# Performance work log

Measured on AMD Instinct MI355X. Metric: run time of the kernel, lower is better.

## Reference

```python
import jax, jax.numpy as jnp
import numpy as np


def setup_inputs() -> dict:
    key = jax.random.key(0)
    k1, k2, k3, k4 = jax.random.split(key, 4)
    N, E, F, H = 100000, 1600000, 128, 128
    x = jax.random.normal(k1, (N, F), dtype=jnp.float32)
    edge_index = jax.random.randint(k2, (2, E), 0, N, dtype=jnp.int64)
    W1 = jax.random.normal(k3, (F, H), dtype=jnp.float32) * (1.0 / np.sqrt(F))
    b1 = jnp.zeros((H,), dtype=jnp.float32)
    W2 = jax.random.normal(k4, (H, H), dtype=jnp.float32) * (1.0 / np.sqrt(H))
    b2 = jnp.zeros((H,), dtype=jnp.float32)
    return {"x": x, "edge_index": edge_index, "W1": W1, "b1": b1, "W2": W2, "b2": b2}


def reference(x, edge_index, W1, b1, W2, b2):
    # Two-layer cached GCN: norm is computed once (cached) and reused by both layers.
    N = x.shape[0]
    loops = jnp.arange(N, dtype=edge_index.dtype)
    src = jnp.concatenate([edge_index[0], loops])  # add self-loops
    dst = jnp.concatenate([edge_index[1], loops])
    # symmetric GCN normalization: deg^-1/2[src] * deg^-1/2[dst]
    deg = jax.ops.segment_sum(jnp.ones_like(dst, dtype=x.dtype), dst, num_segments=N)
    dinv = jnp.where(deg > 0, jax.lax.rsqrt(deg), 0.0)
    norm = dinv[src] * dinv[dst]  # [E+N]

    def conv(h, W, b):
        h = h @ W  # dense transform before sparse aggregate (cheaper: out_dim small)
        msg = norm[:, None] * h[src]  # gather + scale
        return jax.ops.segment_sum(msg, dst, num_segments=N) + b

    h = jax.nn.relu(conv(x, W1, b1))
    # dropout is identity in eval mode (deterministic reference)
    return conv(h, W2, b2)
```

## Files before the change

kernel.cpp:

```cpp
#include <hip/hip_runtime.h>


#define BKT_SHIFT 7
#define BKT_NODES 128
#define CH 8192
#define MAXBKT 1024

typedef _Float16 half4v __attribute__((ext_vector_type(4)));
typedef _Float16 half8v __attribute__((ext_vector_type(8)));
typedef float float4v __attribute__((ext_vector_type(4)));

__global__ __launch_bounds__(256) void k_bincount(const int* __restrict__ dst,
                                                  int* __restrict__ bcnt, int E, int nbkt) {
    __shared__ int sh[MAXBKT];
    for (int i = threadIdx.x; i < nbkt; i += 256) sh[i] = 0;
    __syncthreads();
    for (long long e = (long long)blockIdx.x * 256 + threadIdx.x; e < E;
         e += (long long)gridDim.x * 256)
        atomicAdd(&sh[dst[e] >> BKT_SHIFT], 1);
    __syncthreads();
    for (int i = threadIdx.x; i < nbkt; i += 256)
        if (sh[i]) atomicAdd(&bcnt[i], sh[i]);
}

__global__ __launch_bounds__(1024) void k_bscan(const int* __restrict__ bcnt,
                                                int* __restrict__ bofs,
                                                int* __restrict__ bcur, int nbkt, int E) {
    __shared__ int sh[1024];
    int t = threadIdx.x;
    int v = (t < nbkt) ? bcnt[t] : 0;
    int x = v;
    sh[t] = x;
    __syncthreads();
    for (int o = 1; o < 1024; o <<= 1) {
        int y = (t >= o) ? sh[t - o] : 0;
        __syncthreads();
        x += y;
        sh[t] = x;
        __syncthreads();
    }
    if (t < nbkt) { bofs[t] = x - v; bcur[t] = x - v; }
    if (t == 0) bofs[nbkt] = E;
}

__global__ __launch_bounds__(256) void k_binfill(const int* __restrict__ src,
                                                 const int* __restrict__ dst,
                                                 int* __restrict__ bcur,
                                                 unsigned* __restrict__ recs,
                                                 int E, int nbkt) {
    __shared__ unsigned stage[CH];
    __shared__ unsigned short stageb[CH];
    __shared__ int cnt[MAXBKT];
    __shared__ int base[MAXBKT];
    const int t = threadIdx.x;
    const long long c0 = (long long)blockIdx.x * CH;

    for (int i = t; i < nbkt; i += 256) cnt[i] = 0;
    __syncthreads();

    for (int k = 0; k < CH / 256; k++) {
        int i = k * 256 + t;
        long long e = c0 + i;
        if (e < E) {
            int d = dst[e];
            int b = d >> BKT_SHIFT;
            stage[i] = ((unsigned)(d & (BKT_NODES - 1)) << 17) | (unsigned)src[e];
            stageb[i] = (unsigned short)b;
            atomicAdd(&cnt[b], 1);
        }
    }
    __syncthreads();

    for (int i = t; i < nbkt; i += 256) {
        int c = cnt[i];
        base[i] = c ? atomicAdd(&bcur[i], c) : 0;
        cnt[i] = 0;
    }
    __syncthreads();

    for (int k = 0; k < CH / 256; k++) {
        int i = k * 256 + t;
        if (c0 + i < E) {
            int b = stageb[i];
            int p = base[b] + atomicAdd(&cnt[b], 1);
            recs[p] = stage[i];
        }
    }
}

__global__ __launch_bounds__(256) void k_deg_bins(const unsigned* __restrict__ recs,
                                                  const int* __restrict__ bofs,
                                                  int* __restrict__ deg, int n) {
    __shared__ int cnt[BKT_NODES];
    const int b = blockIdx.x, t = threadIdx.x;
    if (t < BKT_NODES) cnt[t] = 0;
    __syncthreads();
    const int beg = bofs[b], end = bofs[b + 1];
    for (int j = beg + t; j < end; j += 256)
        atomicAdd(&cnt[recs[j] >> 17], 1);
    __syncthreads();
    const int d0 = b << BKT_SHIFT;
    if (t < BKT_NODES && d0 + t < n) deg[d0 + t] = cnt[t];
}

__global__ void k_scan1(const int* __restrict__ deg, float* __restrict__ dinv,
                        int* __restrict__ ofs, int* __restrict__ sums, int n) {
    __shared__ int sh[256];
    const int t = threadIdx.x;
    const int i = blockIdx.x * 256 + t;
    int v = (i < n) ? deg[i] : 0;
    if (i < n) dinv[i] = rsqrtf((float)v + 1.0f);
    int x = v;
    sh[t] = x;
    __syncthreads();
    for (int o = 1; o < 256; o <<= 1) {
        int y = (t >= o) ? sh[t - o] : 0;
        __syncthreads();
        x += y;
        sh[t] = x;
        __syncthreads();
    }
    if (i < n) ofs[i] = x - v;
    if (t == 255) sums[blockIdx.x] = x;
}

__global__ void k_scan2(int* __restrict__ sums, int nb) {
    __shared__ int sh[512];
    const int t = threadIdx.x;
    int carry = 0;
    for (int base = 0; base < nb; base += 512) {
        int i = base + t;
        int v = (i < nb) ? sums[i] : 0;
        int x = v;
        sh[t] = x;
        __syncthreads();
        for (int o = 1; o < 512; o <<= 1) {
            int y = (t >= o) ? sh[t - o] : 0;
            __syncthreads();
            x += y;
            sh[t] = x;
            __syncthreads();
        }
        if (i < nb) sums[i] = x - v + carry;
        int tot = sh[511];
        __syncthreads();
        carry += tot;
    }
}

__global__ void k_scan3(int* __restrict__ ofs, const int* __restrict__ sums, int n, int E) {
    int i = blockIdx.x * 256 + threadIdx.x;
    if (i < n) ofs[i] += sums[blockIdx.x];
    if (i == 0) ofs[n] = E;
}

__global__ __launch_bounds__(256) void k_fill_bins(const unsigned* __restrict__ recs,
                                                   const int* __restrict__ bofs,
                                                   const int* __restrict__ ofs,
                                                   int* __restrict__ col, int n) {
    __shared__ int cur[BKT_NODES];
    const int b = blockIdx.x, t = threadIdx.x;
    const int d0 = b << BKT_SHIFT;
    if (t < BKT_NODES) cur[t] = (d0 + t < n) ? ofs[d0 + t] : 0;
    __syncthreads();
    const int beg = bofs[b], end = bofs[b + 1];
    for (int j = beg + t; j < end; j += 256) {
        unsigned r = recs[j];
        int p = atomicAdd(&cur[r >> 17], 1);
        col[p] = (int)(r & 0x1FFFF);
    }
}

__global__ __launch_bounds__(256) void k_wt(const float* __restrict__ W,
                                            _Float16* __restrict__ Wt) {
    int i = blockIdx.x * 256 + threadIdx.x;
    int k = i >> 7, c = i & 127;
    Wt[c * 128 + k] = (_Float16)W[k * 128 + c];
}

__global__ __launch_bounds__(256, 2) void k_gemm_mfma(const float* __restrict__ in,
                                                      const _Float16* __restrict__ Wt,
                                                      const float* __restrict__ dinv,
                                                      _Float16* __restrict__ out,
                                                      int n, int relu_in) {
    __shared__ _Float16 Al[64][136];
    __shared__ _Float16 Bl[128][136];
    const int t = threadIdx.x;
    const int row0 = blockIdx.x * 64;
    int nr = n - row0;
    if (nr > 64) nr = 64;

    for (int i = t; i < 128 * 16; i += 256) {
        int r = i >> 4, c8 = i & 15;
        *(half8v*)&Bl[r][c8 * 8] = *(const half8v*)&Wt[r * 128 + c8 * 8];
    }
    for (int i = t; i < nr * 32; i += 256) {
        int r = i >> 5, c4 = i & 31;
        float4 v = *(const float4*)&in[(size_t)(row0 + r) * 128 + c4 * 4];
        if (relu_in) {
            v.x = fmaxf(v.x, 0.f); v.y = fmaxf(v.y, 0.f);
            v.z = fmaxf(v.z, 0.f); v.w = fmaxf(v.w, 0.f);
        }
        half4v hv;
        hv[0] = (_Float16)v.x; hv[1] = (_Float16)v.y;
        hv[2] = (_Float16)v.z; hv[3] = (_Float16)v.w;
        *(half4v*)&Al[r][c4 * 4] = hv;
    }
    __syncthreads();

    const int wave = t >> 6;
    const int lane = t & 63;
    const int m0 = wave * 16;
    const int ml = lane & 15;
    const int quad = lane >> 4;

    float4v acc[8] = {};
#pragma unroll
    for (int kc = 0; kc < 4; kc++) {
        half8v a = *(const half8v*)&Al[m0 + ml][kc * 32 + quad * 8];
#pragma unroll
        for (int nt = 0; nt < 8; nt++) {
            half8v b = *(const half8v*)&Bl[nt * 16 + ml][kc * 32 + quad * 8];
            acc[nt] = __builtin_amdgcn_mfma_f32_16x16x32_f16(a, b, acc[nt], 0, 0, 0);
        }
    }

#pragma unroll
    for (int reg = 0; reg < 4; reg++) {
        int r = m0 + quad * 4 + reg;
        if (r < nr) {
            float dv = dinv[row0 + r];
#pragma unroll
            for (int nt = 0; nt < 8; nt++)
                out[(size_t)(row0 + r) * 128 + nt * 16 + ml] =
                    (_Float16)(acc[nt][reg] * dv);
        }
    }
}

__global__ __launch_bounds__(256) void k_agg_csr(const int* __restrict__ ofs,
                                                 const int* __restrict__ col,
                                                 const float* __restrict__ dinv,
                                                 const half4v* __restrict__ ts,
                                                 const float* __restrict__ bias,
                                                 float* __restrict__ out, int n) {
    int gid = blockIdx.x * 256 + threadIdx.x;
    int row = gid >> 5;
    int lane = gid & 31;
    if (row >= n) return;

    float dd = dinv[row];
    int beg = ofs[row];
    int end = ofs[row + 1];

    half4v sv = ts[(size_t)row * 32 + lane];
    float4 acc = make_float4((float)sv[0], (float)sv[1], (float)sv[2], (float)sv[3]);

    int j = beg;
    for (; j + 3 < end; j += 4) {
        int s0 = col[j], s1 = col[j + 1], s2 = col[j + 2], s3 = col[j + 3];
        half4v v0 = ts[(size_t)s0 * 32 + lane];
        half4v v1 = ts[(size_t)s1 * 32 + lane];
        half4v v2 = ts[(size_t)s2 * 32 + lane];
        half4v v3 = ts[(size_t)s3 * 32 + lane];
        acc.x += (float)v0[0] + (float)v1[0] + (float)v2[0] + (float)v3[0];
        acc.y += (float)v0[1] + (float)v1[1] + (float)v2[1] + (float)v3[1];
        acc.z += (float)v0[2] + (float)v1[2] + (float)v2[2] + (float)v3[2];
        acc.w += (float)v0[3] + (float)v1[3] + (float)v2[3] + (float)v3[3];
    }
    for (; j < end; j++) {
        half4v v = ts[(size_t)col[j] * 32 + lane];
        acc.x += (float)v[0];
        acc.y += (float)v[1];
        acc.z += (float)v[2];
        acc.w += (float)v[3];
    }

    float4 bv = *(const float4*)&bias[lane * 4];
    float4 o;
    o.x = bv.x + dd * acc.x;
    o.y = bv.y + dd * acc.y;
    o.z = bv.z + dd * acc.z;
    o.w = bv.w + dd * acc.w;
    *(float4*)&out[(size_t)row * 128 + lane * 4] = o;
}

extern "C" void kernel_launch(void* const* d_in, const int* in_sizes, int n_in,
                              void* d_out, int out_size, void* d_ws, size_t ws_size,
                              hipStream_t stream) {
    const int N = in_sizes[0] / 128;
    const int E = in_sizes[1] / 2;
    const float* x  = (const float*)d_in[0];
    const int*   ei = (const int*)d_in[1];
    const float* W1 = (const float*)d_in[2];
    const float* b1 = (const float*)d_in[3];
    const float* W2 = (const float*)d_in[4];
    const float* b2 = (const float*)d_in[5];

    const int* src = ei;
    const int* dst = ei + E;

    const int nb_n  = (N + 255) / 256;
    const int NBKT  = (N + BKT_NODES - 1) / BKT_NODES;

    _Float16* t    = (_Float16*)d_ws;
    _Float16* wt1  = t + (size_t)N * 128;
    _Float16* wt2  = wt1 + 16384;
    float*    dinv = (float*)(wt2 + 16384);
    int*      ofs  = (int*)(dinv + N);
    int*      deg  = ofs + N + 1;
    int*      sums = deg + N;
    unsigned* recs = (unsigned*)(sums + ((nb_n + 255) & ~255));
    int*      col  = (int*)(recs + E);
    int*      bofs = col + E;
    int*      bcur = bofs + NBKT + 1;
    int*      bcnt = bcur + NBKT;

    float* h   = (float*)d_out;
    float* out = (float*)d_out;

    const int nb_g = (N + 63) / 64;
    const int nb_a = (int)(((long long)N * 32 + 255) / 256);
    const int nb_c = (int)(((long long)E + CH - 1) / CH);

    k_wt<<<64, 256, 0, stream>>>(W1, wt1);
    k_wt<<<64, 256, 0, stream>>>(W2, wt2);
    hipMemsetAsync(bcnt, 0, (size_t)NBKT * 4, stream);
    k_bincount<<<256, 256, 0, stream>>>(dst, bcnt, E, NBKT);
    k_bscan<<<1, 1024, 0, stream>>>(bcnt, bofs, bcur, NBKT, E);
    k_binfill<<<nb_c, 256, 0, stream>>>(src, dst, bcur, recs, E, NBKT);
    k_deg_bins<<<NBKT, 256, 0, stream>>>(recs, bofs, deg, N);
    k_scan1<<<nb_n, 256, 0, stream>>>(deg, dinv, ofs, sums, N);
    k_scan2<<<1, 512, 0, stream>>>(sums, nb_n);
    k_scan3<<<nb_n, 256, 0, stream>>>(ofs, sums, N, E);
    k_fill_bins<<<NBKT, 256, 0, stream>>>(recs, bofs, ofs, col, N);

    k_gemm_mfma<<<nb_g, 256, 0, stream>>>(x, wt1, dinv, t, N, 0);
    k_agg_csr<<<nb_a, 256, 0, stream>>>(ofs, col, dinv, (const half4v*)t, b1, h, N);

    k_gemm_mfma<<<nb_g, 256, 0, stream>>>(h, wt2, dinv, t, N, 1);
    k_agg_csr<<<nb_a, 256, 0, stream>>>(ofs, col, dinv, (const half4v*)t, b2, out, N);
}
```

Before: 345.8 us.

## Fuse degree, scan and CSR fill into one per-bucket kernel; widen aggregation loads

Degree counting, the three-pass global prefix scan and the column fill are merged into a single per-bucket kernel. It derives each node's offset from the bucket base plus a local scan, removing four launches and the deg/sums buffers. The two weight-transpose launches are merged into one. Binfill now uses larger chunks and re-reads dst instead of staging bucket ids in LDS. Aggregation uses 16 lanes per row with 8-half loads, trading more registers per thread for fewer, wider gather requests.

After: 350.4 us. No clear change (+1.3%).

```diff
diff --git a/kernel.cpp b/kernel.cpp
--- a/kernel.cpp
+++ b/kernel.cpp
@@ -3,7 +3,7 @@
 
 #define BKT_SHIFT 7
 #define BKT_NODES 128
-#define CH 8192
+#define CH 12288
 #define MAXBKT 1024
 
 typedef _Float16 half4v __attribute__((ext_vector_type(4)));
@@ -49,7 +49,6 @@
                                                  unsigned* __restrict__ recs,
                                                  int E, int nbkt) {
     __shared__ unsigned stage[CH];
-    __shared__ unsigned short stageb[CH];
     __shared__ int cnt[MAXBKT];
     __shared__ int base[MAXBKT];
     const int t = threadIdx.x;
@@ -63,10 +62,8 @@
         long long e = c0 + i;
         if (e < E) {
             int d = dst[e];
-            int b = d >> BKT_SHIFT;
             stage[i] = ((unsigned)(d & (BKT_NODES - 1)) << 17) | (unsigned)src[e];
-            stageb[i] = (unsigned short)b;
-            atomicAdd(&cnt[b], 1);
+            atomicAdd(&cnt[d >> BKT_SHIFT], 1);
         }
     }
     __syncthreads();
@@ -80,101 +77,72 @@
 
     for (int k = 0; k < CH / 256; k++) {
         int i = k * 256 + t;
-        if (c0 + i < E) {
-            int b = stageb[i];
+        long long e = c0 + i;
+        if (e < E) {
+            int b = dst[e] >> BKT_SHIFT;
             int p = base[b] + atomicAdd(&cnt[b], 1);
             recs[p] = stage[i];
         }
     }
 }
 
-__global__ __launch_bounds__(256) void k_deg_bins(const unsigned* __restrict__ recs,
+__global__ __launch_bounds__(256) void k_csr_bins(const unsigned* __restrict__ recs,
                                                   const int* __restrict__ bofs,
-                                                  int* __restrict__ deg, int n) {
+                                                  float* __restrict__ dinv,
+                                                  int* __restrict__ ofs,
+                                                  int* __restrict__ col, int n, int E) {
     __shared__ int cnt[BKT_NODES];
+    __shared__ int sh[256];
+    __shared__ int cur[BKT_NODES];
     const int b = blockIdx.x, t = threadIdx.x;
+    const int d0 = b << BKT_SHIFT;
     if (t < BKT_NODES) cnt[t] = 0;
     __syncthreads();
     const int beg = bofs[b], end = bofs[b + 1];
     for (int j = beg + t; j < end; j += 256)
         atomicAdd(&cnt[recs[j] >> 17], 1);
     __syncthreads();
-    const int d0 = b << BKT_SHIFT;
-    if (t < BKT_NODES && d0 + t < n) deg[d0 + t] = cnt[t];
-}
-
-__global__ void k_scan1(const int* __restrict__ deg, float* __restrict__ dinv,
-                        int* __restrict__ ofs, int* __restrict__ sums, int n) {
-    __shared__ int sh[256];
-    const int t = threadIdx.x;
-    const int i = blockIdx.x * 256 + t;
-    int v = (i < n) ? deg[i] : 0;
-    if (i < n) dinv[i] = rsqrtf((float)v + 1.0f);
+
+    int v = (t < BKT_NODES) ? cnt[t] : 0;
     int x = v;
     sh[t] = x;
     __syncthreads();
-    for (int o = 1; o < 256; o <<= 1) {
+    for (int o = 1; o < BKT_NODES; o <<= 1) {
         int y = (t >= o) ? sh[t - o] : 0;
         __syncthreads();
         x += y;
         sh[t] = x;
         __syncthreads();
     }
-    if (i < n) ofs[i] = x - v;
-    if (t == 255) sums[blockIdx.x] = x;
-}
-
-__global__ void k_scan2(int* __restrict__ sums, int nb) {
-    __shared__ int sh[512];
-    const int t = threadIdx.x;
-    int carry = 0;
-    for (int base = 0; base < nb; base += 512) {
-        int i = base + t;
-        int v = (i < nb) ? sums[i] : 0;
-        int x = v;
-        sh[t] = x;
-        __syncthreads();
-        for (int o = 1; o < 512; o <<= 1) {
-            int y = (t >= o) ? sh[t - o] : 0;
-            __syncthreads();
-            x += y;
-            sh[t] = x;
-            __syncthreads();
-        }
-        if (i < nb) sums[i] = x - v + carry;
-        int tot = sh[511];
-        __syncthreads();
-        carry += tot;
-    }
-}
-
-__global__ void k_scan3(int* __restrict__ ofs, const int* __restrict__ sums, int n, int E) {
-    int i = blockIdx.x * 256 + threadIdx.x;
-    if (i < n) ofs[i] += sums[blockIdx.x];
-    if (i == 0) ofs[n] = E;
-}
-
-__global__ __launch_bounds__(256) void k_fill_bins(const unsigned* __restrict__ recs,
-                                                   const int* __restrict__ bofs,
-                                                   const int* __restrict__ ofs,
-                                                   int* __restrict__ col, int n) {
-    __shared__ int cur[BKT_NODES];
-    const int b = blockIdx.x, t = threadIdx.x;
-    const int d0 = b << BKT_SHIFT;
-    if (t < BKT_NODES) cur[t] = (d0 + t < n) ? ofs[d0 + t] : 0;
-    __syncthreads();
-    const int beg = bofs[b], end = bofs[b + 1];
+
+    if (t < BKT_NODES) {
+        int node = d0 + t;
+        if (node < n) {
+            int o = beg + (x - v);
+            ofs[node] = o;
+            cur[t] = o;
+            dinv[node] = rsqrtf((float)v + 1.0f);
+        }
+    }
+    __syncthreads();
+
     for (int j = beg + t; j < end; j += 256) {
         unsigned r = recs[j];
         int p = atomicAdd(&cur[r >> 17], 1);
         col[p] = (int)(r & 0x1FFFF);
     }
-}
-
-__global__ __launch_bounds__(256) void k_wt(const float* __restrict__ W,
-                                            _Float16* __restrict__ Wt) {
+    if (b == (int)gridDim.x - 1 && t == 0) ofs[n] = E;
+}
+
+__global__ __launch_bounds__(256) void k_wt2(const float* __restrict__ W1,
+                                             const float* __restrict__ W2,
+                                             _Float16* __restrict__ wt1,
+                                             _Float16* __restrict__ wt2) {
     int i = blockIdx.x * 256 + threadIdx.x;
-    int k = i >> 7, c = i & 127;
+    const float* W = (i < 16384) ? W1 : W2;
+    _Float16* Wt = (i < 16384) ? wt1 : wt2;
+    int j = i & 16383;
+    int k = j >> 7, c = j & 127;
     Wt[c * 128 + k] = (_Float16)W[k * 128 + c];
 }
 
@@ -241,48 +209,49 @@
 __global__ __launch_bounds__(256) void k_agg_csr(const int* __restrict__ ofs,
                                                  const int* __restrict__ col,
                                                  const float* __restrict__ dinv,
-                                                 const half4v* __restrict__ ts,
+                                                 const half8v* __restrict__ ts,
                                                  const float* __restrict__ bias,
                                                  float* __restrict__ out, int n) {
     int gid = blockIdx.x * 256 + threadIdx.x;
-    int row = gid >> 5;
-    int lane = gid & 31;
+    int row = gid >> 4;
+    int lane = gid & 15;
     if (row >= n) return;
 
     float dd = dinv[row];
     int beg = ofs[row];
     int end = ofs[row + 1];
 
-    half4v sv = ts[(size_t)row * 32 + lane];
-    float4 acc = make_float4((float)sv[0], (float)sv[1], (float)sv[2], (float)sv[3]);
+    half8v sv = ts[(size_t)row * 16 + lane];
+    float acc[8];
+#pragma unroll
+    for (int i = 0; i < 8; i++) acc[i] = (float)sv[i];
 
     int j = beg;
     for (; j + 3 < end; j += 4) {
         int s0 = col[j], s1 = col[j + 1], s2 = col[j + 2], s3 = col[j + 3];
-        half4v v0 = ts[(size_t)s0 * 32 + lane];
-        half4v v1 = ts[(size_t)s1 * 32 + lane];
-        half4v v2 = ts[(size_t)s2 * 32 + lane];
-        half4v v3 = ts[(size_t)s3 * 32 + lane];
-        acc.x += (float)v0[0] + (float)v1[0] + (float)v2[0] + (float)v3[0];
-        acc.y += (float)v0[1] + (float)v1[1] + (float)v2[1] + (float)v3[1];
-        acc.z += (float)v0[2] + (float)v1[2] + (float)v2[2] + (float)v3[2];
-        acc.w += (float)v0[3] + (float)v1[3] + (float)v2[3] + (float)v3[3];
+        half8v v0 = ts[(size_t)s0 * 16 + lane];
+        half8v v1 = ts[(size_t)s1 * 16 + lane];
+        half8v v2 = ts[(size_t)s2 * 16 + lane];
+        half8v v3 = ts[(size_t)s3 * 16 + lane];
+#pragma unroll
+        for (int i = 0; i < 8; i++)
+            acc[i] += (float)v0[i] + (float)v1[i] + (float)v2[i] + (float)v3[i];
     }
     for (; j < end; j++) {
-        half4v v = ts[(size_t)col[j] * 32 + lane];
-        acc.x += (float)v[0];
-        acc.y += (float)v[1];
-        acc.z += (float)v[2];
-        acc.w += (float)v[3];
-    }
-
-    float4 bv = *(const float4*)&bias[lane * 4];
-    float4 o;
-    o.x = bv.x + dd * acc.x;
-    o.y = bv.y + dd * acc.y;
-    o.z = bv.z + dd * acc.z;
-    o.w = bv.w + dd * acc.w;
-    *(float4*)&out[(size_t)row * 128 + lane * 4] = o;
+        half8v v = ts[(size_t)col[j] * 16 + lane];
+#pragma unroll
+        for (int i = 0; i < 8; i++) acc[i] += (float)v[i];
+    }
+
+    float4 b0 = *(const float4*)&bias[lane * 8];
+    float4 b1 = *(const float4*)&bias[lane * 8 + 4];
+    float4 o0, o1;
+    o0.x = b0.x + dd * acc[0]; o0.y = b0.y + dd * acc[1];
+    o0.z = b0.z + dd * acc[2]; o0.w = b0.w + dd * acc[3];
+    o1.x = b1.x + dd * acc[4]; o1.y = b1.y + dd * acc[5];
+    o1.z = b1.z + dd * acc[6]; o1.w = b1.w + dd * acc[7];
+    *(float4*)&out[(size_t)row * 128 + lane * 8] = o0;
+    *(float4*)&out[(size_t)row * 128 + lane * 8 + 4] = o1;
 }
 
 extern "C" void kernel_launch(void* const* d_in, const int* in_sizes, int n_in,
@@ -300,17 +269,14 @@
     const int* src = ei;
     const int* dst = ei + E;
 
-    const int nb_n  = (N + 255) / 256;
-    const int NBKT  = (N + BKT_NODES - 1) / BKT_NODES;
+    const int NBKT = (N + BKT_NODES - 1) / BKT_NODES;
 
     _Float16* t    = (_Float16*)d_ws;
     _Float16* wt1  = t + (size_t)N * 128;
     _Float16* wt2  = wt1 + 16384;
     float*    dinv = (float*)(wt2 + 16384);
     int*      ofs  = (int*)(dinv + N);
-    int*      deg  = ofs + N + 1;
-    int*      sums = deg + N;
-    unsigned* recs = (unsigned*)(sums + ((nb_n + 255) & ~255));
+    unsigned* recs = (unsigned*)(ofs + N + 1);
     int*      col  = (int*)(recs + E);
     int*      bofs = col + E;
     int*      bcur = bofs + NBKT + 1;
@@ -320,24 +286,19 @@
     float* out = (float*)d_out;
 
     const int nb_g = (N + 63) / 64;
-    const int nb_a = (int)(((long long)N * 32 + 255) / 256);
+    const int nb_a = (int)(((long long)N * 16 + 255) / 256);
     const int nb_c = (int)(((long long)E + CH - 1) / CH);
 
-    k_wt<<<64, 256, 0, stream>>>(W1, wt1);
-    k_wt<<<64, 256, 0, stream>>>(W2, wt2);
+    k_wt2<<<128, 256, 0, stream>>>(W1, W2, wt1, wt2);
     hipMemsetAsync(bcnt, 0, (size_t)NBKT * 4, stream);
-    k_bincount<<<256, 256, 0, stream>>>(dst, bcnt, E, NBKT);
+    k_bincount<<<64, 256, 0, stream>>>(dst, bcnt, E, NBKT);
     k_bscan<<<1, 1024, 0, stream>>>(bcnt, bofs, bcur, NBKT, E);
     k_binfill<<<nb_c, 256, 0, stream>>>(src, dst, bcur, recs, E, NBKT);
-    k_deg_bins<<<NBKT, 256, 0, stream>>>(recs, bofs, deg, N);
-    k_scan1<<<nb_n, 256, 0, stream>>>(deg, dinv, ofs, sums, N);
-    k_scan2<<<1, 512, 0, stream>>>(sums, nb_n);
-    k_scan3<<<nb_n, 256, 0, stream>>>(ofs, sums, N, E);
-    k_fill_bins<<<NBKT, 256, 0, stream>>>(recs, bofs, ofs, col, N);
+    k_csr_bins<<<NBKT, 256, 0, stream>>>(recs, bofs, dinv, ofs, col, N, E);
 
     k_gemm_mfma<<<nb_g, 256, 0, stream>>>(x, wt1, dinv, t, N, 0);
-    k_agg_csr<<<nb_a, 256, 0, stream>>>(ofs, col, dinv, (const half4v*)t, b1, h, N);
+    k_agg_csr<<<nb_a, 256, 0, stream>>>(ofs, col, dinv, (const half8v*)t, b1, h, N);
 
     k_gemm_mfma<<<nb_g, 256, 0, stream>>>(h, wt2, dinv, t, N, 1);
-    k_agg_csr<<<nb_a, 256, 0, stream>>>(ofs, col, dinv, (const half4v*)t, b2, out, N);
-}
+    k_agg_csr<<<nb_a, 256, 0, stream>>>(ofs, col, dinv, (const half8v*)t, b2, out, N);
+}
```
